# Kernel optimization log

Hardware: AMD Instinct MI355X
Metric: run time of the kernel (lower is better)

Reference implementation:

```python
import jax, jax.numpy as jnp
import numpy as np
from jax import lax

B, T = 64, 512
CHAR_V, BICHAR_V, EMB = 10000, 200000, 128
E = 2 * EMB          # concat of char + bichar embeddings
H = 384              # LSTM hidden size per direction
K = 13               # num tags


def setup_inputs() -> dict:
    key = jax.random.key(0)
    ks = jax.random.split(key, 16)
    s = 0.05
    char_id = jax.random.randint(ks[0], (B, T), 0, CHAR_V)
    bichar_id = jax.random.randint(ks[1], (B, T), 0, BICHAR_V)
    label_id = jax.random.randint(ks[2], (B, T), 0, K)
    char_table = (jax.random.normal(ks[3], (CHAR_V, EMB), jnp.float32) * s).at[0].set(0.0)  # padding_idx=0
    bichar_table = (jax.random.normal(ks[4], (BICHAR_V, EMB), jnp.float32) * s).at[0].set(0.0)
    w_ih_f = jax.random.normal(ks[5], (4 * H, E), jnp.float32) * s
    w_hh_f = jax.random.normal(ks[6], (4 * H, H), jnp.float32) * s
    b_f = jax.random.normal(ks[7], (4 * H,), jnp.float32) * s     # b_ih + b_hh combined
    w_ih_b = jax.random.normal(ks[8], (4 * H, E), jnp.float32) * s
    w_hh_b = jax.random.normal(ks[9], (4 * H, H), jnp.float32) * s
    b_b = jax.random.normal(ks[10], (4 * H,), jnp.float32) * s
    w_em = jax.random.normal(ks[11], (K, 2 * H), jnp.float32) * s
    b_em = jax.random.normal(ks[12], (K,), jnp.float32) * s
    start_trans = jax.random.normal(ks[13], (K,), jnp.float32) * s
    end_trans = jax.random.normal(ks[14], (K,), jnp.float32) * s
    trans = jax.random.normal(ks[15], (K, K), jnp.float32) * s
    return dict(char_id=char_id, bichar_id=bichar_id, label_id=label_id,
                char_table=char_table, bichar_table=bichar_table,
                w_ih_f=w_ih_f, w_hh_f=w_hh_f, b_f=b_f,
                w_ih_b=w_ih_b, w_hh_b=w_hh_b, b_b=b_b,
                w_em=w_em, b_em=b_em,
                start_trans=start_trans, end_trans=end_trans, trans=trans)


def _lstm(x, w_ih, w_hh, b, reverse):
    # x: [B, T, E] -> hidden states [B, T, H].  PyTorch gate order: i, f, g, o.
    Bx = x.shape[0]
    xg = jnp.einsum('bte,ge->btg', x, w_ih) + b  # precompute input projections [B,T,4H]
    def step(carry, xg_t):
        h, c = carry
        g = xg_t + h @ w_hh.T
        i, f, gg, o = jnp.split(g, 4, axis=-1)
        c = jax.nn.sigmoid(f) * c + jax.nn.sigmoid(i) * jnp.tanh(gg)
        h = jax.nn.sigmoid(o) * jnp.tanh(c)
        return (h, c), h
    h0 = jnp.zeros((Bx, H), x.dtype)
    _, hs = lax.scan(step, (h0, h0), xg.transpose(1, 0, 2), reverse=reverse)
    return hs.transpose(1, 0, 2)


def _crf_nll(emissions, tags, mask, start_trans, end_trans, trans):
    # pytorch-crf negative log-likelihood, reduction='mean'. emissions [B,T,K].
    Bx = emissions.shape[0]
    mf = mask.astype(emissions.dtype)
    bidx = jnp.arange(Bx)
    # numerator: score of the gold tag sequence
    t0 = tags[:, 0]
    score = start_trans[t0] + emissions[bidx, 0, t0]
    trans_sc = trans[tags[:, :-1], tags[:, 1:]]                                # [B,T-1]
    em_sc = jnp.take_along_axis(emissions[:, 1:], tags[:, 1:, None], axis=2)[..., 0]
    score = score + jnp.sum((trans_sc + em_sc) * mf[:, 1:], axis=1)
    seq_ends = jnp.sum(mask, axis=1).astype(jnp.int32) - 1
    score = score + end_trans[tags[bidx, seq_ends]]
    # denominator: forward algorithm (log-domain DP over time)
    alpha0 = start_trans[None, :] + emissions[:, 0]                            # [B,K]
    def step(alpha, inp):
        em_t, m_t = inp                                                        # [B,K], [B]
        nxt = jax.nn.logsumexp(alpha[:, :, None] + trans[None] + em_t[:, None, :], axis=1)
        return jnp.where(m_t[:, None], nxt, alpha), None
    alpha, _ = lax.scan(step, alpha0,
                        (emissions[:, 1:].transpose(1, 0, 2), mask[:, 1:].T))
    logZ = jax.nn.logsumexp(alpha + end_trans[None, :], axis=1)
    llh = score - logZ
    return -jnp.mean(llh)


def reference(char_id, bichar_id, label_id, char_table, bichar_table,
              w_ih_f, w_hh_f, b_f, w_ih_b, w_hh_b, b_b,
              w_em, b_em, start_trans, end_trans, trans):
    # embeddings + concat (dropout is identity in eval/reference)
    chars = jnp.concatenate([char_table[char_id], bichar_table[bichar_id]], axis=-1)  # [B,T,2*EMB]
    h_fwd = _lstm(chars, w_ih_f, w_hh_f, b_f, reverse=False)
    h_bwd = _lstm(chars, w_ih_b, w_hh_b, b_b, reverse=True)
    sen = jnp.concatenate([h_fwd, h_bwd], axis=-1)                                    # [B,T,2H]
    emission = jax.nn.log_softmax(jnp.einsum('bth,kh->btk', sen, w_em) + b_em, axis=-1)
    bio_mask = char_id != 0
    return _crf_nll(emission, label_id, bio_mask, start_trans, end_trans, trans)
```

## Files before the change

### kernel.cpp

```cpp
#include <hip/hip_runtime.h>
#include <math.h>

#define B_    64
#define T_    512
#define EMB_  128
#define E_    256
#define H_    384
#define K_    13
#define NBG   4
#define NG    6
#define NW    8
#define XROWB 1296

typedef short s8v __attribute__((ext_vector_type(8)));
typedef short s4v __attribute__((ext_vector_type(4)));
typedef float f4v __attribute__((ext_vector_type(4)));
typedef unsigned long long ull;

__device__ __forceinline__ float sigm(float x){ return 1.f/(1.f+__expf(-x)); }
__device__ __forceinline__ float tanh_f(float x){ return 2.f/(1.f+__expf(-2.f*x)) - 1.f; }
__device__ __forceinline__ short f2bf(float x){
  unsigned u = __builtin_bit_cast(unsigned, x);
  return (short)((u + 0x7FFFu + ((u>>16)&1u)) >> 16);
}
__device__ __forceinline__ float bf2f(short s){
  return __builtin_bit_cast(float, ((unsigned)(unsigned short)s) << 16);
}
__device__ __forceinline__ size_t hslot(int par, int dir, int bg){
  return (size_t)(((par*2 + dir)*NBG + bg)) * (NG*16*64);
}
#define LBAR() do{ __builtin_amdgcn_sched_barrier(0); \
  asm volatile("s_waitcnt lgkmcnt(0)" ::: "memory"); \
  __builtin_amdgcn_s_barrier(); \
  __builtin_amdgcn_sched_barrier(0); }while(0)

__global__ __launch_bounds__(256) void k_packA(
    const float* __restrict__ wih_f, const float* __restrict__ whh_f,
    const float* __restrict__ wih_b, const float* __restrict__ whh_b,
    s8v* __restrict__ Apack)
{
  int idx = blockIdx.x*256 + threadIdx.x;
  if (idx >= 12*NW*2*20*64) return;
  int l   = idx & 63;
  int f   = idx >> 6;
  int kt  = f % 20;
  int rt  = (f/20) & 1;
  int w   = (f/40) % NW;
  int set = f/(40*NW);
  int g   = set % NG, dir = set / NG;
  const float* wih = dir ? wih_b : wih_f;
  const float* whh = dir ? whh_b : whh_f;
  int pr = l & 15;
  int R  = (pr&3)*H_ + g*64 + (w*8 + rt*4 + (pr>>2));
  int kb = kt*32 + (l>>4)*8;
  const float* src;
  if (kb < E_) src = wih + (size_t)R*E_ + kb;
  else         src = whh + (size_t)R*H_ + ((g*64 + kb - E_) % H_);
  s8v out;
  #pragma unroll
  for (int e = 0; e < 8; e++) out[e] = f2bf(src[e]);
  Apack[idx] = out;
}

__global__ __launch_bounds__(256) void k_embX(
    const int* __restrict__ char_id, const int* __restrict__ bichar_id,
    const float* __restrict__ char_table, const float* __restrict__ bichar_table,
    short* __restrict__ X_all)
{
  int rid  = blockIdx.x*4 + (threadIdx.x>>6);
  int lane = threadIdx.x & 63;
  int t = rid >> 6, b = rid & 63;
  float4 v;
  if (lane < 32) { int c = char_id  [b*T_ + t]; v = *(const float4*)(char_table  + (size_t)c*EMB_ + lane*4); }
  else           { int c = bichar_id[b*T_ + t]; v = *(const float4*)(bichar_table+ (size_t)c*EMB_ + (lane-32)*4); }
  s4v o; o[0]=f2bf(v.x); o[1]=f2bf(v.y); o[2]=f2bf(v.z); o[3]=f2bf(v.w);
  *(s4v*)(X_all + ((size_t)rid*E_ + lane*4)) = o;
}

__global__ __launch_bounds__(512, 2) void k_lstm_p(
    const s8v* __restrict__ Apack,
    const short* __restrict__ X_all,
    const float* __restrict__ b_f, const float* __restrict__ b_b,
    const float* __restrict__ w_em,
    unsigned* __restrict__ h_slot,
    short* __restrict__ em16)
{
  __shared__ char  Xsb[16*XROWB];
  __shared__ short hsl[16][66];
  __shared__ float wems[K_][64];

  const int bid = blockIdx.x;
  const int dir = bid & 1, bg = (bid>>1)&3, g = bid>>3;
  const int tid = threadIdx.x, lane = tid & 63, w = tid >> 6;
  const int pb  = (dir*NBG+bg)*NG + g;

  s8v fr0[20], fr1[20];
  {
    const s8v* ap = Apack + ((size_t)((dir*NG+g)*NW + w)*40)*64 + lane;
    #pragma unroll
    for (int kt = 0; kt < 20; kt++) fr0[kt] = ap[kt*64];
    #pragma unroll
    for (int kt = 0; kt < 20; kt++) fr1[kt] = ap[(20+kt)*64];
  }
  for (int i = tid; i < K_*64; i += 512)
    wems[i>>6][i&63] = w_em[(size_t)(i>>6)*(2*H_) + dir*H_ + g*64 + (i&63)];

  const int batch = lane & 15;
  const int uA = w*8 + (lane>>4), uB = uA + 4;
  const float* bias = dir ? b_b : b_f;
  float bA[4], bB[4];
  #pragma unroll
  for (int r = 0; r < 4; r++) { bA[r] = bias[r*H_ + g*64 + uA]; bB[r] = bias[r*H_ + g*64 + uB]; }
  float cA = 0.f, cB = 0.f;

  const int b_x = tid>>5, kox = (tid&31)*8;
  const int b_r = tid>>5, ch = tid&31;
  int poff[5];
  int posb[5];
  #pragma unroll
  for (int i = 0; i < 5; i++) {
    int p = (g + 1 + i) % NG;
    poff[i] = (p*16 + b_r)*64 + ch*2;
    posb[i] = ((p - g + NG) % NG) * 64 + ch*2;
  }

  for (int cc = tid; cc < 16*192; cc += 512)
    *(unsigned*)(Xsb + (cc/192)*XROWB + 512 + (cc%192)*4) = 0u;

  s8v xv = *(const s8v*)(X_all + ((size_t)((dir?(T_-1):0)*B_ + bg*16 + b_x)*E_ + kox));
  __syncthreads();

  for (int s = 0; s < T_; s++) {
    const int t  = dir ? (T_-1-s) : s;
    const int tp = dir ? t+1 : t-1;
    const int tn = dir ? t-1 : t+1;

    *(s8v*)(Xsb + b_x*XROWB + 2*kox) = xv;
    if (s+1 < T_) xv = *(const s8v*)(X_all + ((size_t)(tn*B_ + bg*16 + b_x)*E_ + kox));

    LBAR();

    if (s > 0) {
      for (int k = w; k < K_; k += NW) {
        int b = lane>>2, cq = lane&3;
        float acc = 0.f;
        #pragma unroll
        for (int m = 0; m < 8; m++) {
          int u = cq*16 + 2*m;
          unsigned pr = *(const unsigned*)&hsl[b][u];
          acc += bf2f((short)(pr & 0xFFFF)) * wems[k][u]
               + bf2f((short)(pr >> 16))    * wems[k][u+1];
        }
        acc += __shfl_xor(acc, 1, 64);
        acc += __shfl_xor(acc, 2, 64);
        if (cq == 0) em16[((size_t)(pb*T_ + tp)*16 + b)*K_ + k] = f2bf(acc);
      }
    }

    f4v a0 = {0.f,0.f,0.f,0.f}, a1 = a0;
    #pragma unroll
    for (int kt = 0; kt < 10; kt++) {
      s8v bq = *(const s8v*)(Xsb + (lane&15)*XROWB + kt*64 + (lane>>4)*16);
      a0 = __builtin_amdgcn_mfma_f32_16x16x32_bf16(fr0[kt], bq, a0, 0,0,0);
      a1 = __builtin_amdgcn_mfma_f32_16x16x32_bf16(fr1[kt], bq, a1, 0,0,0);
    }

    if (s > 0) {
      const unsigned tag = (unsigned)(tp & 0xFFFF);
      const ull tagpair = (ull)tag | ((ull)tag << 32);
      const unsigned* vb = h_slot + hslot(tp&1, dir, bg);
      ull v0, v1, v2, v3, v4;
      int tr = 0;
      while (true) {
        v0 = __hip_atomic_load((const ull*)(vb + poff[0]), __ATOMIC_RELAXED, __HIP_MEMORY_SCOPE_AGENT);
        v1 = __hip_atomic_load((const ull*)(vb + poff[1]), __ATOMIC_RELAXED, __HIP_MEMORY_SCOPE_AGENT);
        v2 = __hip_atomic_load((const ull*)(vb + poff[2]), __ATOMIC_RELAXED, __HIP_MEMORY_SCOPE_AGENT);
        v3 = __hip_atomic_load((const ull*)(vb + poff[3]), __ATOMIC_RELAXED, __HIP_MEMORY_SCOPE_AGENT);
        v4 = __hip_atomic_load((const ull*)(vb + poff[4]), __ATOMIC_RELAXED, __HIP_MEMORY_SCOPE_AGENT);
        ull m = (v0^tagpair) | (v1^tagpair) | (v2^tagpair) | (v3^tagpair) | (v4^tagpair);
        if ((m & 0x0000FFFF0000FFFFull) == 0ull) break;
        if (++tr > 16) __builtin_amdgcn_s_sleep(1);
      }
      ull vv[5] = {v0, v1, v2, v3, v4};
      #pragma unroll
      for (int i = 0; i < 5; i++) {
        unsigned lo = (unsigned)vv[i], hi = (unsigned)(vv[i] >> 32);
        *(unsigned*)(Xsb + b_r*XROWB + 512 + posb[i]*2) = (lo >> 16) | (hi & 0xFFFF0000u);
      }
    }
    LBAR();

    #pragma unroll
    for (int kt = 10; kt < 20; kt++) {
      s8v bq = *(const s8v*)(Xsb + (lane&15)*XROWB + kt*64 + (lane>>4)*16);
      a0 = __builtin_amdgcn_mfma_f32_16x16x32_bf16(fr0[kt], bq, a0, 0,0,0);
      a1 = __builtin_amdgcn_mfma_f32_16x16x32_bf16(fr1[kt], bq, a1, 0,0,0);
    }

    {
      cA = sigm(a0[1]+bA[1])*cA + sigm(a0[0]+bA[0])*tanh_f(a0[2]+bA[2]);
      float h0 = sigm(a0[3]+bA[3])*tanh_f(cA);
      cB = sigm(a1[1]+bB[1])*cB + sigm(a1[0]+bB[0])*tanh_f(a1[2]+bB[2]);
      float h1 = sigm(a1[3]+bB[3])*tanh_f(cB);
      short hb0 = f2bf(h0), hb1 = f2bf(h1);
      unsigned vt = (unsigned)(t & 0xFFFF);
      unsigned q0 = ((unsigned)(unsigned short)hb0 << 16) | vt;
      unsigned q1 = ((unsigned)(unsigned short)hb1 << 16) | vt;
      unsigned* hw = h_slot + hslot(t&1, dir, bg) + (size_t)(g*16 + batch)*64;
      __hip_atomic_store(hw + uA, q0, __ATOMIC_RELAXED, __HIP_MEMORY_SCOPE_AGENT);
      __hip_atomic_store(hw + uB, q1, __ATOMIC_RELAXED, __HIP_MEMORY_SCOPE_AGENT);
      *(short*)(Xsb + batch*XROWB + 512 + uA*2) = hb0;
      *(short*)(Xsb + batch*XROWB + 512 + uB*2) = hb1;
      hsl[batch][uA] = hb0;
      hsl[batch][uB] = hb1;
    }
  }

  LBAR();
  {
    const int tl = dir ? 0 : T_-1;
    for (int k = w; k < K_; k += NW) {
      int b = lane>>2, cq = lane&3;
      float acc = 0.f;
      #pragma unroll
      for (int m = 0; m < 8; m++) {
        int u = cq*16 + 2*m;
        unsigned pr = *(const unsigned*)&hsl[b][u];
        acc += bf2f((short)(pr & 0xFFFF)) * wems[k][u]
             + bf2f((short)(pr >> 16))    * wems[k][u+1];
      }
      acc += __shfl_xor(acc, 1, 64);
      acc += __shfl_xor(acc, 2, 64);
      if (cq == 0) em16[((size_t)(pb*T_ + tl)*16 + b)*K_ + k] = f2bf(acc);
    }
  }
}

__global__ __launch_bounds__(256) void k_em2(
    const short* __restrict__ em16, const float* __restrict__ b_em,
    float* __restrict__ em)
{
  int r = blockIdx.x*256 + threadIdx.x;
  int b = r >> 9, t = r & 511;
  int bg = b >> 4, b16 = b & 15;
  float e[K_];
  #pragma unroll
  for (int k = 0; k < K_; k++) e[k] = b_em[k];
  #pragma unroll
  for (int dir = 0; dir < 2; dir++)
    for (int g = 0; g < NG; g++) {
      int pb = (dir*NBG+bg)*NG + g;
      const short* p = em16 + ((size_t)(pb*T_ + t)*16 + b16)*K_;
      #pragma unroll
      for (int k = 0; k < K_; k++) e[k] += bf2f(p[k]);
    }
  float mx = -1e30f;
  #pragma unroll
  for (int k = 0; k < K_; k++) mx = fmaxf(mx, e[k]);
  float S = 0.f;
  #pragma unroll
  for (int k = 0; k < K_; k++) S += __expf(e[k]-mx);
  float L = __logf(S) + mx;
  #pragma unroll
  for (int k = 0; k < K_; k++) em[(size_t)r*K_+k] = e[k] - L;
}

__global__ __launch_bounds__(64) void k_crf(
    const int* __restrict__ char_id, const int* __restrict__ label_id,
    const float* __restrict__ em,
    const float* __restrict__ start_trans, const float* __restrict__ end_trans,
    const float* __restrict__ trans, float* __restrict__ llh)
{
  int b = blockIdx.x, lane = threadIdx.x;
  const int*   cid = char_id  + b*T_;
  const int*   tag = label_id + b*T_;
  const float* emb = em + (size_t)b*T_*K_;

  float sc = 0.f; int cntm = 0;
  for (int t = lane; t < T_; t += 64) {
    int m = (cid[t] != 0);
    cntm += m;
    if (t >= 1 && m) sc += trans[tag[t-1]*K_ + tag[t]] + emb[t*K_ + tag[t]];
  }
  #pragma unroll
  for (int off = 32; off; off >>= 1) { sc += __shfl_xor(sc, off, 64); cntm += __shfl_xor(cntm, off, 64); }

  __shared__ float alpha[K_];
  __shared__ float scoreSh;
  if (lane == 0) {
    int t0 = tag[0];
    int ce = (cntm > 0) ? (cntm - 1) : 0;
    scoreSh = start_trans[t0] + emb[t0] + sc + end_trans[tag[ce]];
  }
  if (lane < K_) alpha[lane] = start_trans[lane] + emb[lane];
  float tr[K_];
  if (lane < K_) {
    #pragma unroll
    for (int i = 0; i < K_; i++) tr[i] = trans[i*K_ + lane];
  }
  __syncthreads();

  for (int t = 1; t < T_; t++) {
    bool mt = (cid[t] != 0);
    float nxt = 0.f;
    if (lane < K_) {
      float a[K_];
      #pragma unroll
      for (int i = 0; i < K_; i++) a[i] = alpha[i] + tr[i];
      float m = a[0];
      #pragma unroll
      for (int i = 1; i < K_; i++) m = fmaxf(m, a[i]);
      float s2 = 0.f;
      #pragma unroll
      for (int i = 0; i < K_; i++) s2 += __expf(a[i]-m);
      nxt = m + __logf(s2) + emb[t*K_ + lane];
    }
    __syncthreads();
    if (lane < K_ && mt) alpha[lane] = nxt;
    __syncthreads();
  }

  if (lane == 0) {
    float m = alpha[0] + end_trans[0];
    #pragma unroll
    for (int k = 1; k < K_; k++) m = fmaxf(m, alpha[k]+end_trans[k]);
    float s2 = 0.f;
    #pragma unroll
    for (int k = 0; k < K_; k++) s2 += __expf(alpha[k]+end_trans[k]-m);
    llh[b] = scoreSh - (m + __logf(s2));
  }
}

__global__ __launch_bounds__(64) void k_final(const float* __restrict__ llh, float* __restrict__ out){
  float v = llh[threadIdx.x];
  #pragma unroll
  for (int off = 32; off; off >>= 1) v += __shfl_xor(v, off, 64);
  if (threadIdx.x == 0) out[0] = -v / (float)B_;
}

extern "C" void kernel_launch(void* const* d_in, const int* in_sizes, int n_in,
                              void* d_out, int out_size, void* d_ws, size_t ws_size,
                              hipStream_t stream)
{
  const int*   char_id      = (const int*)  d_in[0];
  const int*   bichar_id    = (const int*)  d_in[1];
  const int*   label_id     = (const int*)  d_in[2];
  const float* char_table   = (const float*)d_in[3];
  const float* bichar_table = (const float*)d_in[4];
  const float* w_ih_f       = (const float*)d_in[5];
  const float* w_hh_f       = (const float*)d_in[6];
  const float* b_f          = (const float*)d_in[7];
  const float* w_ih_b       = (const float*)d_in[8];
  const float* w_hh_b       = (const float*)d_in[9];
  const float* b_b          = (const float*)d_in[10];
  const float* w_em         = (const float*)d_in[11];
  const float* b_em         = (const float*)d_in[12];
  const float* start_trans  = (const float*)d_in[13];
  const float* end_trans    = (const float*)d_in[14];
  const float* trans        = (const float*)d_in[15];

  char* w = (char*)d_ws;
  s8v*      Apack  = (s8v*)w;      w += (size_t)12*NW*2*20*64*16;
  short*    X_all  = (short*)w;    w += (size_t)T_*B_*E_*2;
  unsigned* h_slot = (unsigned*)w; w += (size_t)2*2*NBG*NG*16*64*4;
  short*    em16   = (short*)w;    w += (size_t)48*T_*16*K_*2;
  float*    em_out = (float*)w;    w += (size_t)B_*T_*K_*4;
  float*    llh    = (float*)w;    w += 256;

  hipMemsetAsync(h_slot, 0xFF, (size_t)2*2*NBG*NG*16*64*4, stream);

  k_packA<<<960, 256, 0, stream>>>(w_ih_f, w_hh_f, w_ih_b, w_hh_b, Apack);
  k_embX <<<8192, 256, 0, stream>>>(char_id, bichar_id, char_table, bichar_table, X_all);
  k_lstm_p<<<48, 512, 0, stream>>>(Apack, X_all, b_f, b_b, w_em, h_slot, em16);
  k_em2  <<<128, 256, 0, stream>>>(em16, b_em, em_out);
  k_crf  <<<64, 64, 0, stream>>>(char_id, label_id, em_out, start_trans, end_trans, trans, llh);
  k_final<<<1, 64, 0, stream>>>(llh, (float*)d_out);
}
```

Baseline: 1.664 ms.

## Place LSTM chain blocks per XCC and exchange hidden state via XCC-local L2

Launches 256 blocks, and each block reads its XCC id through a hardware register and claims a (chain, group) role with an atomic counter. This places all six cooperating blocks of one recurrence chain on the same XCC, and surplus blocks exit. The hidden-state exchange now writes to a fast buffer with workgroup scope and reads it with sc0 loads, so the traffic is meant to stay in the shared XCC L2 instead of going to device-coherent memory. A second copy is written at agent scope as a fallback that pollers switch to after repeated spin failures. This relies on undocumented placement behaviour, and correctness depends on the fallback path when blocks do not share an XCC.

```diff
diff --git a/kernel.cpp b/kernel.cpp
--- a/kernel.cpp
+++ b/kernel.cpp
@@ -82,16 +82,29 @@
     const short* __restrict__ X_all,
     const float* __restrict__ b_f, const float* __restrict__ b_b,
     const float* __restrict__ w_em,
-    unsigned* __restrict__ h_slot,
+    unsigned* __restrict__ h_fast,
+    unsigned* __restrict__ h_safe,
+    int* __restrict__ claim,
     short* __restrict__ em16)
 {
   __shared__ char  Xsb[16*XROWB];
   __shared__ short hsl[16][66];
   __shared__ float wems[K_][64];
-
-  const int bid = blockIdx.x;
-  const int dir = bid & 1, bg = (bid>>1)&3, g = bid>>3;
+  __shared__ int   roleSh[2];
+
   const int tid = threadIdx.x, lane = tid & 63, w = tid >> 6;
+
+  if (tid == 0) {
+    unsigned xcc;
+    asm volatile("s_getreg_b32 %0, hwreg(HW_REG_XCC_ID)" : "=s"(xcc));
+    int chain = (int)(xcc & 7u);
+    int idx = atomicAdd(&claim[chain], 1);
+    roleSh[0] = chain; roleSh[1] = idx;
+  }
+  __syncthreads();
+  const int chain = roleSh[0], ridx = roleSh[1];
+  if (ridx >= NG) return;
+  const int dir = chain & 1, bg = chain >> 1, g = ridx;
   const int pb  = (dir*NBG+bg)*NG + g;
 
   s8v fr0[20], fr1[20];
@@ -123,6 +136,7 @@
     poff[i] = (p*16 + b_r)*64 + ch*2;
     posb[i] = ((p - g + NG) % NG) * 64 + ch*2;
   }
+  bool useSafe = false;
 
   for (int cc = tid; cc < 16*192; cc += 512)
     *(unsigned*)(Xsb + (cc/192)*XROWB + 512 + (cc%192)*4) = 0u;
@@ -168,18 +182,36 @@
     if (s > 0) {
       const unsigned tag = (unsigned)(tp & 0xFFFF);
       const ull tagpair = (ull)tag | ((ull)tag << 32);
-      const unsigned* vb = h_slot + hslot(tp&1, dir, bg);
+      const unsigned* fb = h_fast + hslot(tp&1, dir, bg);
+      const unsigned* sb = h_safe + hslot(tp&1, dir, bg);
       ull v0, v1, v2, v3, v4;
       int tr = 0;
       while (true) {
-        v0 = __hip_atomic_load((const ull*)(vb + poff[0]), __ATOMIC_RELAXED, __HIP_MEMORY_SCOPE_AGENT);
-        v1 = __hip_atomic_load((const ull*)(vb + poff[1]), __ATOMIC_RELAXED, __HIP_MEMORY_SCOPE_AGENT);
-        v2 = __hip_atomic_load((const ull*)(vb + poff[2]), __ATOMIC_RELAXED, __HIP_MEMORY_SCOPE_AGENT);
-        v3 = __hip_atomic_load((const ull*)(vb + poff[3]), __ATOMIC_RELAXED, __HIP_MEMORY_SCOPE_AGENT);
-        v4 = __hip_atomic_load((const ull*)(vb + poff[4]), __ATOMIC_RELAXED, __HIP_MEMORY_SCOPE_AGENT);
+        if (!useSafe) {
+          asm volatile(
+            "global_load_dwordx2 %0, %5, off sc0\n\t"
+            "global_load_dwordx2 %1, %6, off sc0\n\t"
+            "global_load_dwordx2 %2, %7, off sc0\n\t"
+            "global_load_dwordx2 %3, %8, off sc0\n\t"
+            "global_load_dwordx2 %4, %9, off sc0\n\t"
+            "s_waitcnt vmcnt(0)"
+            : "=v"(v0), "=v"(v1), "=v"(v2), "=v"(v3), "=v"(v4)
+            : "v"((const ull*)(fb + poff[0])), "v"((const ull*)(fb + poff[1])),
+              "v"((const ull*)(fb + poff[2])), "v"((const ull*)(fb + poff[3])),
+              "v"((const ull*)(fb + poff[4]))
+            : "memory");
+        } else {
+          v0 = __hip_atomic_load((const ull*)(sb + poff[0]), __ATOMIC_RELAXED, __HIP_MEMORY_SCOPE_AGENT);
+          v1 = __hip_atomic_load((const ull*)(sb + poff[1]), __ATOMIC_RELAXED, __HIP_MEMORY_SCOPE_AGENT);
+          v2 = __hip_atomic_load((const ull*)(sb + poff[2]), __ATOMIC_RELAXED, __HIP_MEMORY_SCOPE_AGENT);
+          v3 = __hip_atomic_load((const ull*)(sb + poff[3]), __ATOMIC_RELAXED, __HIP_MEMORY_SCOPE_AGENT);
+          v4 = __hip_atomic_load((const ull*)(sb + poff[4]), __ATOMIC_RELAXED, __HIP_MEMORY_SCOPE_AGENT);
+        }
         ull m = (v0^tagpair) | (v1^tagpair) | (v2^tagpair) | (v3^tagpair) | (v4^tagpair);
         if ((m & 0x0000FFFF0000FFFFull) == 0ull) break;
-        if (++tr > 16) __builtin_amdgcn_s_sleep(1);
+        ++tr;
+        if (tr > 64) useSafe = true;
+        if (tr > 16) __builtin_amdgcn_s_sleep(1);
       }
       ull vv[5] = {v0, v1, v2, v3, v4};
       #pragma unroll
@@ -206,9 +238,11 @@
       unsigned vt = (unsigned)(t & 0xFFFF);
       unsigned q0 = ((unsigned)(unsigned short)hb0 << 16) | vt;
       unsigned q1 = ((unsigned)(unsigned short)hb1 << 16) | vt;
-      unsigned* hw = h_slot + hslot(t&1, dir, bg) + (size_t)(g*16 + batch)*64;
-      __hip_atomic_store(hw + uA, q0, __ATOMIC_RELAXED, __HIP_MEMORY_SCOPE_AGENT);
-      __hip_atomic_store(hw + uB, q1, __ATOMIC_RELAXED, __HIP_MEMORY_SCOPE_AGENT);
+      size_t off = hslot(t&1, dir, bg) + (size_t)(g*16 + batch)*64;
+      __hip_atomic_store(h_fast + off + uA, q0, __ATOMIC_RELAXED, __HIP_MEMORY_SCOPE_WORKGROUP);
+      __hip_atomic_store(h_fast + off + uB, q1, __ATOMIC_RELAXED, __HIP_MEMORY_SCOPE_WORKGROUP);
+      __hip_atomic_store(h_safe + off + uA, q0, __ATOMIC_RELAXED, __HIP_MEMORY_SCOPE_AGENT);
+      __hip_atomic_store(h_safe + off + uB, q1, __ATOMIC_RELAXED, __HIP_MEMORY_SCOPE_AGENT);
       *(short*)(Xsb + batch*XROWB + 512 + uA*2) = hb0;
       *(short*)(Xsb + batch*XROWB + 512 + uB*2) = hb1;
       hsl[batch][uA] = hb0;
@@ -362,16 +396,19 @@
   char* w = (char*)d_ws;
   s8v*      Apack  = (s8v*)w;      w += (size_t)12*NW*2*20*64*16;
   short*    X_all  = (short*)w;    w += (size_t)T_*B_*E_*2;
-  unsigned* h_slot = (unsigned*)w; w += (size_t)2*2*NBG*NG*16*64*4;
+  unsigned* h_fast = (unsigned*)w; w += (size_t)2*2*NBG*NG*16*64*4;
+  unsigned* h_safe = (unsigned*)w; w += (size_t)2*2*NBG*NG*16*64*4;
+  int*      claim  = (int*)w;      w += 512;
   short*    em16   = (short*)w;    w += (size_t)48*T_*16*K_*2;
   float*    em_out = (float*)w;    w += (size_t)B_*T_*K_*4;
   float*    llh    = (float*)w;    w += 256;
 
-  hipMemsetAsync(h_slot, 0xFF, (size_t)2*2*NBG*NG*16*64*4, stream);
+  hipMemsetAsync(h_fast, 0xFF, (size_t)2 * (2*2*NBG*NG*16*64*4), stream);
+  hipMemsetAsync(claim, 0, 512, stream);
 
   k_packA<<<960, 256, 0, stream>>>(w_ih_f, w_hh_f, w_ih_b, w_hh_b, Apack);
   k_embX <<<8192, 256, 0, stream>>>(char_id, bichar_id, char_table, bichar_table, X_all);
-  k_lstm_p<<<48, 512, 0, stream>>>(Apack, X_all, b_f, b_b, w_em, h_slot, em16);
+  k_lstm_p<<<256, 512, 0, stream>>>(Apack, X_all, b_f, b_b, w_em, h_fast, h_safe, claim, em16);
   k_em2  <<<128, 256, 0, stream>>>(em16, b_em, em_out);
   k_crf  <<<64, 64, 0, stream>>>(char_id, label_id, em_out, start_trans, end_trans, trans, llh);
   k_final<<<1, 64, 0, stream>>>(llh, (float*)d_out);
```

Result: slower. 2.064 ms (+24.0%).

## Transpose h exchange buffer to unit-major and make CRF forward register-resident

Applied to the files above, without the earlier changes.

The global hidden-state exchange buffer changes from batch-major to unit-major, so each thread's 64-bit polling load covers two batches for one unit at contiguous per-thread addresses, and the stores and LDS scatter are rewritten to match. Separately, the CRF forward recursion keeps alpha in registers and broadcasts it with shuffles plus an online logsumexp, replacing the shared-memory round trip and two block barriers per timestep. The intent is to cut inter-block h exchange latency and serial CRF overhead. The cost is scattered 32-bit stores into the new layout and LDS writes that are now 16-bit instead of 32-bit.

```diff
diff --git a/kernel.cpp b/kernel.cpp
--- a/kernel.cpp
+++ b/kernel.cpp
@@ -27,7 +27,7 @@
   return __builtin_bit_cast(float, ((unsigned)(unsigned short)s) << 16);
 }
 __device__ __forceinline__ size_t hslot(int par, int dir, int bg){
-  return (size_t)(((par*2 + dir)*NBG + bg)) * (NG*16*64);
+  return (size_t)(((par*2 + dir)*NBG + bg)) * (NG*64*16);
 }
 #define LBAR() do{ __builtin_amdgcn_sched_barrier(0); \
   asm volatile("s_waitcnt lgkmcnt(0)" ::: "memory"); \
@@ -114,14 +114,15 @@
   float cA = 0.f, cB = 0.f;
 
   const int b_x = tid>>5, kox = (tid&31)*8;
-  const int b_r = tid>>5, ch = tid&31;
-  int poff[5];
+  const int u_l = tid >> 3;
+  const int b0  = (tid & 7) * 2;
+  int pidx[5];
   int posb[5];
   #pragma unroll
   for (int i = 0; i < 5; i++) {
     int p = (g + 1 + i) % NG;
-    poff[i] = (p*16 + b_r)*64 + ch*2;
-    posb[i] = ((p - g + NG) % NG) * 64 + ch*2;
+    pidx[i] = p*512 + tid;
+    posb[i] = ((p - g + NG) % NG) * 64 + u_l;
   }
 
   for (int cc = tid; cc < 16*192; cc += 512)
@@ -168,15 +169,15 @@
     if (s > 0) {
       const unsigned tag = (unsigned)(tp & 0xFFFF);
       const ull tagpair = (ull)tag | ((ull)tag << 32);
-      const unsigned* vb = h_slot + hslot(tp&1, dir, bg);
+      const ull* vb = (const ull*)(h_slot + hslot(tp&1, dir, bg));
       ull v0, v1, v2, v3, v4;
       int tr = 0;
       while (true) {
-        v0 = __hip_atomic_load((const ull*)(vb + poff[0]), __ATOMIC_RELAXED, __HIP_MEMORY_SCOPE_AGENT);
-        v1 = __hip_atomic_load((const ull*)(vb + poff[1]), __ATOMIC_RELAXED, __HIP_MEMORY_SCOPE_AGENT);
-        v2 = __hip_atomic_load((const ull*)(vb + poff[2]), __ATOMIC_RELAXED, __HIP_MEMORY_SCOPE_AGENT);
-        v3 = __hip_atomic_load((const ull*)(vb + poff[3]), __ATOMIC_RELAXED, __HIP_MEMORY_SCOPE_AGENT);
-        v4 = __hip_atomic_load((const ull*)(vb + poff[4]), __ATOMIC_RELAXED, __HIP_MEMORY_SCOPE_AGENT);
+        v0 = __hip_atomic_load(vb + pidx[0], __ATOMIC_RELAXED, __HIP_MEMORY_SCOPE_AGENT);
+        v1 = __hip_atomic_load(vb + pidx[1], __ATOMIC_RELAXED, __HIP_MEMORY_SCOPE_AGENT);
+        v2 = __hip_atomic_load(vb + pidx[2], __ATOMIC_RELAXED, __HIP_MEMORY_SCOPE_AGENT);
+        v3 = __hip_atomic_load(vb + pidx[3], __ATOMIC_RELAXED, __HIP_MEMORY_SCOPE_AGENT);
+        v4 = __hip_atomic_load(vb + pidx[4], __ATOMIC_RELAXED, __HIP_MEMORY_SCOPE_AGENT);
         ull m = (v0^tagpair) | (v1^tagpair) | (v2^tagpair) | (v3^tagpair) | (v4^tagpair);
         if ((m & 0x0000FFFF0000FFFFull) == 0ull) break;
         if (++tr > 16) __builtin_amdgcn_s_sleep(1);
@@ -185,7 +186,8 @@
       #pragma unroll
       for (int i = 0; i < 5; i++) {
         unsigned lo = (unsigned)vv[i], hi = (unsigned)(vv[i] >> 32);
-        *(unsigned*)(Xsb + b_r*XROWB + 512 + posb[i]*2) = (lo >> 16) | (hi & 0xFFFF0000u);
+        *(short*)(Xsb + (b0  )*XROWB + 512 + posb[i]*2) = (short)(lo >> 16);
+        *(short*)(Xsb + (b0+1)*XROWB + 512 + posb[i]*2) = (short)(hi >> 16);
       }
     }
     LBAR();
@@ -206,9 +208,11 @@
       unsigned vt = (unsigned)(t & 0xFFFF);
       unsigned q0 = ((unsigned)(unsigned short)hb0 << 16) | vt;
       unsigned q1 = ((unsigned)(unsigned short)hb1 << 16) | vt;
-      unsigned* hw = h_slot + hslot(t&1, dir, bg) + (size_t)(g*16 + batch)*64;
-      __hip_atomic_store(hw + uA, q0, __ATOMIC_RELAXED, __HIP_MEMORY_SCOPE_AGENT);
-      __hip_atomic_store(hw + uB, q1, __ATOMIC_RELAXED, __HIP_MEMORY_SCOPE_AGENT);
+      unsigned* hw = h_slot + hslot(t&1, dir, bg);
+      __hip_atomic_store(hw + (size_t)(g*64 + uA)*16 + batch, q0,
+                         __ATOMIC_RELAXED, __HIP_MEMORY_SCOPE_AGENT);
+      __hip_atomic_store(hw + (size_t)(g*64 + uB)*16 + batch, q1,
+                         __ATOMIC_RELAXED, __HIP_MEMORY_SCOPE_AGENT);
       *(short*)(Xsb + batch*XROWB + 512 + uA*2) = hb0;
       *(short*)(Xsb + batch*XROWB + 512 + uB*2) = hb1;
       hsl[batch][uA] = hb0;
@@ -284,51 +288,42 @@
   }
   #pragma unroll
   for (int off = 32; off; off >>= 1) { sc += __shfl_xor(sc, off, 64); cntm += __shfl_xor(cntm, off, 64); }
-
-  __shared__ float alpha[K_];
-  __shared__ float scoreSh;
+  float score = 0.f;
   if (lane == 0) {
     int t0 = tag[0];
     int ce = (cntm > 0) ? (cntm - 1) : 0;
-    scoreSh = start_trans[t0] + emb[t0] + sc + end_trans[tag[ce]];
-  }
-  if (lane < K_) alpha[lane] = start_trans[lane] + emb[lane];
-  float tr[K_];
-  if (lane < K_) {
-    #pragma unroll
-    for (int i = 0; i < K_; i++) tr[i] = trans[i*K_ + lane];
-  }
-  __syncthreads();
+    score = start_trans[t0] + emb[t0] + sc + end_trans[tag[ce]];
+  }
+
+  int k = (lane < K_) ? lane : 0;
+  float tr_reg[K_];
+  #pragma unroll
+  for (int i = 0; i < K_; i++) tr_reg[i] = trans[i*K_ + k];
+  float alpha = start_trans[k] + emb[k];
 
   for (int t = 1; t < T_; t++) {
     bool mt = (cid[t] != 0);
-    float nxt = 0.f;
-    if (lane < K_) {
-      float a[K_];
-      #pragma unroll
-      for (int i = 0; i < K_; i++) a[i] = alpha[i] + tr[i];
-      float m = a[0];
-      #pragma unroll
-      for (int i = 1; i < K_; i++) m = fmaxf(m, a[i]);
-      float s2 = 0.f;
-      #pragma unroll
-      for (int i = 0; i < K_; i++) s2 += __expf(a[i]-m);
-      nxt = m + __logf(s2) + emb[t*K_ + lane];
-    }
-    __syncthreads();
-    if (lane < K_ && mt) alpha[lane] = nxt;
-    __syncthreads();
-  }
-
-  if (lane == 0) {
-    float m = alpha[0] + end_trans[0];
-    #pragma unroll
-    for (int k = 1; k < K_; k++) m = fmaxf(m, alpha[k]+end_trans[k]);
-    float s2 = 0.f;
-    #pragma unroll
-    for (int k = 0; k < K_; k++) s2 += __expf(alpha[k]+end_trans[k]-m);
-    llh[b] = scoreSh - (m + __logf(s2));
-  }
+    float em_t = emb[t*K_ + k];
+    float m = -1e30f, s = 0.f;
+    #pragma unroll
+    for (int i = 0; i < K_; i++) {
+      float v = __shfl(alpha, i, 64) + tr_reg[i];
+      float nm = fmaxf(m, v);
+      s = s*__expf(m - nm) + __expf(v - nm);
+      m = nm;
+    }
+    float nxt = m + __logf(s) + em_t;
+    if (mt) alpha = nxt;
+  }
+
+  float v  = (lane < K_) ? alpha + end_trans[lane] : -1e30f;
+  float mx = v;
+  #pragma unroll
+  for (int off = 32; off; off >>= 1) mx = fmaxf(mx, __shfl_xor(mx, off, 64));
+  float s2 = __expf(v - mx);
+  #pragma unroll
+  for (int off = 32; off; off >>= 1) s2 += __shfl_xor(s2, off, 64);
+  if (lane == 0) llh[b] = score - (mx + __logf(s2));
 }
 
 __global__ __launch_bounds__(64) void k_final(const float* __restrict__ llh, float* __restrict__ out){
@@ -362,12 +357,12 @@
   char* w = (char*)d_ws;
   s8v*      Apack  = (s8v*)w;      w += (size_t)12*NW*2*20*64*16;
   short*    X_all  = (short*)w;    w += (size_t)T_*B_*E_*2;
-  unsigned* h_slot = (unsigned*)w; w += (size_t)2*2*NBG*NG*16*64*4;
+  unsigned* h_slot = (unsigned*)w; w += (size_t)2*2*NBG*NG*64*16*4;
   short*    em16   = (short*)w;    w += (size_t)48*T_*16*K_*2;
   float*    em_out = (float*)w;    w += (size_t)B_*T_*K_*4;
   float*    llh    = (float*)w;    w += 256;
 
-  hipMemsetAsync(h_slot, 0xFF, (size_t)2*2*NBG*NG*16*64*4, stream);
+  hipMemsetAsync(h_slot, 0xFF, (size_t)2*2*NBG*NG*64*16*4, stream);
 
   k_packA<<<960, 256, 0, stream>>>(w_ih_f, w_hh_f, w_ih_b, w_hh_b, Apack);
   k_embX <<<8192, 256, 0, stream>>>(char_id, bichar_id, char_table, bichar_table, X_all);
```

New measurement: 1.603 ms. -3.7%, faster.
